# Performance work log

Measured on AMD Instinct MI355X. Metric: run time of the kernel, lower is better.

## Reference

```python
import jax, jax.numpy as jnp
import numpy as np
import math

D = 1024
H = 16
DH = D // H


def sinusoidal_pe(length, d):
    pos = jnp.arange(length, dtype=jnp.float32)[:, None]            # [S,1]
    div = jnp.exp(jnp.arange(0, d, 2, dtype=jnp.float32) * (-math.log(10000.0) / d))  # [d/2]
    ang = pos * div                                                  # [S,d/2]
    # interleave sin (even idx) and cos (odd idx)
    return jnp.stack([jnp.sin(ang), jnp.cos(ang)], axis=-1).reshape(length, d)


def setup_inputs() -> dict:
    key = jax.random.key(0)
    ks = jax.random.split(key, 12)
    s = 0.02
    x = jax.random.normal(ks[0], (2, 2048, D), dtype=jnp.float32)
    return {
        "x": x,
        "ln_g": jnp.ones((D,), jnp.float32),
        "ln_b": jnp.zeros((D,), jnp.float32),
        "Wq": jax.random.normal(ks[1], (D, D), jnp.float32) * s,
        "bq": jnp.zeros((D,), jnp.float32),
        "Wk": jax.random.normal(ks[2], (D, D), jnp.float32) * s,
        "bk": jnp.zeros((D,), jnp.float32),
        "Wv": jax.random.normal(ks[3], (D, D), jnp.float32) * s,
        "bv": jnp.zeros((D,), jnp.float32),
        "Wp": jax.random.normal(ks[4], (D, D), jnp.float32) * s,
        "Wo": jax.random.normal(ks[5], (D, D), jnp.float32) * s,
        "bo": jnp.zeros((D,), jnp.float32),
        "u_bias": jax.random.normal(ks[6], (H, DH), jnp.float32) * 0.05,
        "v_bias": jax.random.normal(ks[7], (H, DH), jnp.float32) * 0.05,
    }


def _relative_shift(pos_score):
    # pos_score: [B,H,S,S]
    B, Hh, S1, S2 = pos_score.shape
    padded = jnp.concatenate([jnp.zeros((B, Hh, S1, 1), pos_score.dtype), pos_score], axis=-1)
    padded = padded.reshape(B, Hh, S2 + 1, S1)
    return padded[:, :, 1:].reshape(B, Hh, S1, S2)


def reference(x, ln_g, ln_b, Wq, bq, Wk, bk, Wv, bv, Wp, Wo, bo, u_bias, v_bias):
    B, S, Dm = x.shape
    dh = Dm // H
    scale = dh ** -0.5

    pe = sinusoidal_pe(S, Dm)                                        # [S,D]

    mu = jnp.mean(x, axis=-1, keepdims=True)
    var = jnp.var(x, axis=-1, keepdims=True)
    xn = (x - mu) / jnp.sqrt(var + 1e-5) * ln_g + ln_b

    q = (xn @ Wq + bq).reshape(B, S, H, dh)                          # [B,S,H,dh]
    k = (xn @ Wk + bk).reshape(B, S, H, dh)
    v = (xn @ Wv + bv).reshape(B, S, H, dh)
    p = (pe @ Wp).reshape(S, H, dh)                                  # [S,H,dh]

    content = jnp.einsum('bihd,bjhd->bhij', q + u_bias, k)
    pos = jnp.einsum('bihd,jhd->bhij', q + v_bias, p)
    pos = _relative_shift(pos)

    attn = jax.nn.softmax((content + pos) * scale, axis=-1)          # [B,H,S,S]
    head = jnp.einsum('bhij,bjhd->bihd', attn, v).reshape(B, S, Dm)
    return head @ Wo + bo
```

## Files before the change

kernel.cpp:

```cpp
#include <hip/hip_runtime.h>
#include <hip/hip_bf16.h>
#include <math.h>

#define Dm   1024
#define Hh   16
#define Sx   2048

typedef short s16x8 __attribute__((ext_vector_type(8)));
typedef float f32x4 __attribute__((ext_vector_type(4)));
typedef unsigned short u16;
typedef u16 u16x4 __attribute__((ext_vector_type(4)));

#if defined(__has_builtin)
#  if __has_builtin(__builtin_amdgcn_cvt_pk_bf16_f32)
#    define HAVE_PKBF16 1
typedef __bf16 bfv2 __attribute__((ext_vector_type(2)));
#  endif
#  if __has_builtin(__builtin_amdgcn_exp2f)
#    define EXP2(x) __builtin_amdgcn_exp2f(x)
#  endif
#endif
#ifndef EXP2
#  define EXP2(x) exp2f(x)
#endif

#define ATT_SCALE 0.1803368801111204f

#define BARRIER_LGKM() asm volatile("s_waitcnt lgkmcnt(0)\n\ts_barrier" ::: "memory")

__device__ __forceinline__ float wave_sum64(float v) {
#pragma unroll
    for (int o = 32; o > 0; o >>= 1) v += __shfl_xor(v, o, 64);
    return v;
}
__device__ __forceinline__ u16 f2bf(float x) {
    unsigned int u = __float_as_uint(x);
    unsigned int r = u + 0x7FFFu + ((u >> 16) & 1u);
    return (u16)(r >> 16);
}
__device__ __forceinline__ float bf2f(u16 h) {
    return __uint_as_float(((unsigned int)h) << 16);
}
__device__ __forceinline__ f32x4 mfma16(s16x8 a, s16x8 b, f32x4 c) {
    return __builtin_amdgcn_mfma_f32_16x16x32_bf16(a, b, c, 0, 0, 0);
}
__device__ __forceinline__ void gl16(const u16* gp, u16* lp) {
    __builtin_amdgcn_global_load_lds(
        (__attribute__((address_space(1))) void*)(gp),
        (__attribute__((address_space(3))) void*)(lp), 16, 0, 0);
}

__global__ __launch_bounds__(256) void ln_kernel(const float* __restrict__ x,
                                                 const float* __restrict__ g,
                                                 const float* __restrict__ b,
                                                 u16* __restrict__ out16) {
    int row = blockIdx.x;
    int tid = threadIdx.x;
    const float4* xr = (const float4*)(x + (size_t)row * Dm);
    float4 v = xr[tid];
    float s  = v.x + v.y + v.z + v.w;
    float ss = v.x * v.x + v.y * v.y + v.z * v.z + v.w * v.w;
    __shared__ float rbuf[8];
    s  = wave_sum64(s);
    ss = wave_sum64(ss);
    if ((tid & 63) == 0) { rbuf[tid >> 6] = s; rbuf[4 + (tid >> 6)] = ss; }
    __syncthreads();
    float mean = (rbuf[0] + rbuf[1] + rbuf[2] + rbuf[3]) * (1.0f / Dm);
    float msq  = (rbuf[4] + rbuf[5] + rbuf[6] + rbuf[7]) * (1.0f / Dm);
    float var  = msq - mean * mean;
    float rstd = 1.0f / sqrtf(var + 1e-5f);
    float4 gg = ((const float4*)g)[tid];
    float4 bb = ((const float4*)b)[tid];
    float o[4];
    o[0] = (v.x - mean) * rstd * gg.x + bb.x;
    o[1] = (v.y - mean) * rstd * gg.y + bb.y;
    o[2] = (v.z - mean) * rstd * gg.z + bb.z;
    o[3] = (v.w - mean) * rstd * gg.w + bb.w;
    u16x4 hi, lo;
#pragma unroll
    for (int i = 0; i < 4; i++) {
        u16 h = f2bf(o[i]);
        hi[i] = h;
        lo[i] = f2bf(o[i] - bf2f(h));
    }
    *(u16x4*)&out16[(size_t)row * 2048 + tid * 4]        = hi;
    *(u16x4*)&out16[(size_t)row * 2048 + 1024 + tid * 4] = lo;
}

__global__ __launch_bounds__(256) void pe_kernel(u16* __restrict__ pe16) {
    int idx = blockIdx.x * 256 + threadIdx.x;
    int r = idx >> 9;
    int t = idx & 511;
    float div = expf((float)(2 * t) * (-9.210340371976184f / 1024.0f));
    float ang = (float)r * div;
    float sv, cv;
    sincosf(ang, &sv, &cv);
    u16 sh = f2bf(sv), chh = f2bf(cv);
    u16* row = pe16 + (size_t)r * 2048;
    row[2 * t]            = sh;
    row[2 * t + 1]        = chh;
    row[1024 + 2 * t]     = f2bf(sv - bf2f(sh));
    row[1024 + 2 * t + 1] = f2bf(cv - bf2f(chh));
}

__global__ __launch_bounds__(256) void wconv_kernel(const float* __restrict__ W0,
                                                    const float* __restrict__ W1,
                                                    const float* __restrict__ W2,
                                                    const float* __restrict__ W3,
                                                    const float* __restrict__ W4,
                                                    u16* __restrict__ WT) {
    int wz = blockIdx.z;
    const float* W = (wz == 0) ? W0 : (wz == 1) ? W1 : (wz == 2) ? W2 : (wz == 3) ? W3 : W4;
    u16* T = WT + (size_t)wz * 1024 * 2048;
    __shared__ float tile[32][33];
    int n0 = blockIdx.x * 32, k0 = blockIdx.y * 32;
    int tx = threadIdx.x & 31, ty = threadIdx.x >> 5;
#pragma unroll
    for (int r = 0; r < 32; r += 8)
        tile[ty + r][tx] = W[(size_t)(k0 + ty + r) * 1024 + n0 + tx];
    __syncthreads();
#pragma unroll
    for (int r = 0; r < 32; r += 8) {
        int n = ty + r;
        float x = tile[tx][n];
        u16 h = f2bf(x);
        float rem = x - bf2f(h);
        T[(size_t)(n0 + n) * 2048 + k0 + tx]        = h;
        T[(size_t)(n0 + n) * 2048 + 1024 + k0 + tx] = f2bf(rem);
    }
}

template<int BMT>
__global__ __launch_bounds__(256, 4) void gemm128k(const u16* __restrict__ A,
                                                   const u16* __restrict__ A2,
                                                   const u16* __restrict__ WT,
                                                   const float* __restrict__ b0,
                                                   const float* __restrict__ b1,
                                                   const float* __restrict__ b2,
                                                   const float* __restrict__ ubv,
                                                   const float* __restrict__ vbv,
                                                   float* __restrict__ ukg,
                                                   float* __restrict__ vbg,
                                                   u16* __restrict__ Cb,
                                                   u16* __restrict__ VT,
                                                   float* __restrict__ C,
                                                   int mode) {
    constexpr int MT  = BMT / 32;
    constexpr int AC  = BMT / 32;
    constexpr int RPW = BMT / 4;
    __shared__ __align__(16) u16 AhL[BMT * 64];
    __shared__ __align__(16) u16 BhL[128 * 64];
    int tid = threadIdx.x;
    int gx, gy, widx;
    const u16* Asrc = A;
    if (mode == 0) {
        int bid = blockIdx.x;
        if (bid < 768) { gx = bid % 24; gy = bid / 24; widx = gx >> 3; gx &= 7; }
        else           { int r2 = bid - 768; gx = r2 & 7; gy = r2 >> 3; widx = 3; Asrc = A2; }
    } else {
        gx = blockIdx.x; gy = blockIdx.y; widx = 4;
    }
    int bn = gx * 128, bm = gy * BMT;
    const u16* Wb = WT + (size_t)widx * (1024 * 2048);
    const float* bias = (widx == 0) ? b0 : (widx == 1) ? b1 : (widx == 2) ? b2
                      : (widx == 4) ? b0 : nullptr;
    float csc = (widx == 1 || widx == 3) ? ATT_SCALE : 1.0f;

    int w = tid >> 6, ln = tid & 63, g = ln >> 4, l15 = ln & 15;
    int wm = (w & 1) * (BMT / 2), wn = (w >> 1) * 64;

    int key = ln >> 3;
    int cg  = (ln & 7) ^ key;
    int gcol = (cg < 4) ? cg * 8 : 1024 + (cg - 4) * 8;
    const u16* gA = Asrc + (size_t)(bm + w * RPW + key) * 2048 + gcol;
    const u16* gB = Wb   + (size_t)(bn + w * 32  + key) * 2048 + gcol;
    u16* lA = &AhL[(w * RPW) * 64];
    u16* lB = &BhL[(w * 32) * 64];

    int keyr = l15 & 7;
    int chH = (g ^ keyr) * 8;
    int chL = ((4 + g) ^ keyr) * 8;

    f32x4 acc[MT][4] = {};

    for (int k0 = 0; k0 < 1024; k0 += 32) {
#pragma unroll
        for (int c = 0; c < AC; c++)
            gl16(gA + c * (8 * 2048) + k0, lA + c * (8 * 64));
#pragma unroll
        for (int c = 0; c < 4; c++)
            gl16(gB + c * (8 * 2048) + k0, lB + c * (8 * 64));
        __syncthreads();

        s16x8 bhf[4], blf[4];
#pragma unroll
        for (int nt = 0; nt < 4; nt++) {
            int br = (wn + nt * 16 + l15) * 64;
            bhf[nt] = *(const s16x8*)&BhL[br + chH];
            blf[nt] = *(const s16x8*)&BhL[br + chL];
        }
#pragma unroll
        for (int mt = 0; mt < MT; mt++) {
            int ar = (wm + mt * 16 + l15) * 64;
            s16x8 ah = *(const s16x8*)&AhL[ar + chH];
            s16x8 al = *(const s16x8*)&AhL[ar + chL];
#pragma unroll
            for (int nt = 0; nt < 4; nt++) {
                acc[mt][nt] = mfma16(ah, bhf[nt], acc[mt][nt]);
                acc[mt][nt] = mfma16(al, bhf[nt], acc[mt][nt]);
                acc[mt][nt] = mfma16(ah, blf[nt], acc[mt][nt]);
            }
        }
        __syncthreads();
    }

    float bv4[4];
#pragma unroll
    for (int nt = 0; nt < 4; nt++)
        bv4[nt] = bias ? bias[bn + wn + nt * 16 + l15] : 0.0f;
    if (mode == 0) {
        if (widx == 2) {
            int bb  = bm >> 11;
            int hh  = (bn + wn) >> 6;
            int jt0 = ((bm & 2047) + wm) >> 5;
            int jr0 = g * 4;
#pragma unroll
            for (int mt = 0; mt < MT; mt++) {
#pragma unroll
                for (int nt = 0; nt < 4; nt++) {
                    u16x4 ov;
#pragma unroll
                    for (int r = 0; r < 4; r++)
                        ov[r] = f2bf(acc[mt][nt][r] + bv4[nt]);
                    int jt = jt0 + (mt >> 1);
                    int d  = 16 * nt + l15;
                    u16* dst = VT + ((size_t)(bb * 16 + hh) * 64 + jt) * 2048
                                  + d * 32 + (mt & 1) * 16 + jr0;
                    *(u16x4*)dst = ov;
                }
            }
        } else {
            u16* Co = Cb + (size_t)widx * (4096 * 1024);
            bool dored = (widx == 1 || widx == 3);
            int hh = (bn + wn) >> 6;
            float u4[4] = {0.f, 0.f, 0.f, 0.f};
            if (dored) {
                const float* uv = (widx == 1) ? ubv : vbv;
#pragma unroll
                for (int nt = 0; nt < 4; nt++) u4[nt] = uv[hh * 64 + 16 * nt + l15];
            }
#pragma unroll
            for (int mt = 0; mt < MT; mt++)
#pragma unroll
                for (int r = 0; r < 4; r++) {
                    int row = bm + wm + mt * 16 + g * 4 + r;
                    u16* cp = Co + (size_t)row * 1024 + bn + wn + l15;
                    u16 hv[4];
#pragma unroll
                    for (int nt = 0; nt < 4; nt++) {
                        hv[nt] = f2bf((acc[mt][nt][r] + bv4[nt]) * csc);
                        cp[16 * nt] = hv[nt];
                    }
                    if (dored) {
                        float s = bf2f(hv[0]) * u4[0] + bf2f(hv[1]) * u4[1]
                                + bf2f(hv[2]) * u4[2] + bf2f(hv[3]) * u4[3];
#pragma unroll
                        for (int o = 1; o < 16; o <<= 1) s += __shfl_xor(s, o, 64);
                        if (l15 == 0) {
                            if (widx == 1)
                                ukg[((size_t)((bm >> 11) * 16 + hh)) * 2048
                                    + ((bm & 2047) + wm + mt * 16 + g * 4 + r)] = s;
                            else
                                vbg[(size_t)hh * 2048 + (bm + wm + mt * 16 + g * 4 + r)] = s;
                        }
                    }
                }
        }
    } else {
#pragma unroll
        for (int mt = 0; mt < MT; mt++)
#pragma unroll
            for (int r = 0; r < 4; r++) {
                int row = bm + wm + mt * 16 + g * 4 + r;
                float* cp = C + (size_t)row * 1024 + bn + wn + l15;
#pragma unroll
                for (int nt = 0; nt < 4; nt++)
                    cp[16 * nt] = acc[mt][nt][r] + bv4[nt];
            }
    }
}

__device__ __forceinline__ void wfill2(s16x8 a0, s16x8 a1, const u16* PW,
                                       int g, int l15, f32x4& d0, f32x4& d1) {
    f32x4 z = {0.f, 0.f, 0.f, 0.f};
    s16x8 b00 = *(const s16x8*)&PW[l15 * 72 + g * 8];
    s16x8 b01 = *(const s16x8*)&PW[l15 * 72 + 32 + g * 8];
    s16x8 b10 = *(const s16x8*)&PW[(16 + l15) * 72 + g * 8];
    s16x8 b11 = *(const s16x8*)&PW[(16 + l15) * 72 + 32 + g * 8];
    d0 = mfma16(a0, b00, z);
    d0 = mfma16(a1, b01, d0);
    d1 = mfma16(a0, b10, z);
    d1 = mfma16(a1, b11, d1);
}

__device__ __forceinline__ void window_fill(s16x8 aq0, s16x8 aq1, s16x8 ab0, s16x8 ab1,
                                            const u16* PW, float* Ws,
                                            const float* __restrict__ vbb,
                                            int vstart, int sb, int rbase, int g, int l15) {
    f32x4 e0, e1;
    if (vstart + 31 <= Sx) {
        wfill2(aq0, aq1, PW, g, l15, e0, e1);
    } else if (vstart > Sx) {
        wfill2(ab0, ab1, PW, g, l15, e0, e1);
    } else {
        f32x4 d0, d1, f0, f1;
        wfill2(aq0, aq1, PW, g, l15, d0, d1);
        wfill2(ab0, ab1, PW, g, l15, f0, f1);
        int v0 = vstart + l15, v1 = vstart + 16 + l15;
#pragma unroll
        for (int r = 0; r < 4; r++) {
            e0[r] = (v0 > Sx) ? f0[r] : d0[r];
            e1[r] = (v1 > Sx) ? f1[r] : d1[r];
        }
    }
    int v0 = vstart + l15, v1 = vstart + 16 + l15;
    int pc0 = v0 < Sx ? v0 : v0 - Sx - 1;
    int pc1 = v1 < Sx ? v1 : v1 - Sx - 1;
    float vb0 = (v0 == Sx) ? 0.0f : vbb[pc0];
    float vb1 = (v1 == Sx) ? 0.0f : vbb[pc1];
    int bs = sb + rbase;
#pragma unroll
    for (int r = 0; r < 4; r++) {
        int b2 = bs + r; if (b2 >= 96) b2 -= 96;
        int sl0 = b2 + l15; if (sl0 >= 96) sl0 -= 96;
        int sl1 = sl0 + 16; if (sl1 >= 96) sl1 -= 96;
        Ws[(rbase + r) * 98 + sl0] = (v0 == Sx) ? 0.0f : e0[r] + vb0;
        Ws[(rbase + r) * 98 + sl1] = (v1 == Sx) ? 0.0f : e1[r] + vb1;
    }
}

__global__ __launch_bounds__(256, 4) void flash_kernel(const u16* __restrict__ q,
                                                       const u16* __restrict__ k,
                                                       const u16* __restrict__ vt,
                                                       const u16* __restrict__ pp,
                                                       const float* __restrict__ ukg,
                                                       const float* __restrict__ vbg,
                                                       u16* __restrict__ head16) {
    __shared__ __align__(16) unsigned char smem[39424];
    float* Ws = (float*)smem;
    u16*   Qs = (u16*)smem;
    u16*   Kt = (u16*)(smem + 25088);
    u16*   PW = (u16*)(smem + 29696);
    u16*   PA = (u16*)(smem + 34304);

    int tid = threadIdx.x, blk = blockIdx.x;
    int grp = (blk & 7) + 8 * (blk >> 8);
    int it  = (blk >> 3) & 31;
    int h = grp & 15, b = grp >> 4;
    int i0 = it * 64;
    int a0 = 1984 - i0;

    const u16* qb  = q  + ((size_t)b * Sx) * Dm + h * 64;
    const u16* kb  = k  + ((size_t)b * Sx) * Dm + h * 64;
    const u16* vtb = vt + ((size_t)(b * 16 + h) * 64) * 2048;
    const u16* ppb = pp + h * 64;
    const float* ukb = ukg + (size_t)(b * Hh + h) * Sx;
    const float* vbb = vbg + (size_t)h * Sx;

    int w = tid >> 6, ln = tid & 63, g = ln >> 4, l15 = ln & 15;
    int rv = tid >> 3, ch = tid & 7;
    int rbase = 16 * w + 4 * g;

    for (int c = tid; c < 65 * 8; c += 256) {
        int row = c >> 3, cc = c & 7;
        int i = i0 + row;
        s16x8 tv = {0, 0, 0, 0, 0, 0, 0, 0};
        if (i < Sx) tv = *(const s16x8*)(qb + (size_t)i * Dm + cc * 8);
        *(s16x8*)&Qs[row * 72 + cc * 8] = tv;
    }
    __syncthreads();

    s16x8 aq0 = *(const s16x8*)&Qs[(16 * w + l15) * 72 + g * 8];
    s16x8 aq1 = *(const s16x8*)&Qs[(16 * w + l15) * 72 + 32 + g * 8];
    s16x8 ab0 = *(const s16x8*)&Qs[(16 * w + 1 + l15) * 72 + g * 8];
    s16x8 ab1 = *(const s16x8*)&Qs[(16 * w + 1 + l15) * 72 + 32 + g * 8];
    __syncthreads();

    for (int f = 0; f < 3; f++) {
        int vrb = f * 32;
        if (f) __syncthreads();
        {
            int vv = a0 + vrb + rv;
            s16x8 tv = {0, 0, 0, 0, 0, 0, 0, 0};
            if (vv != Sx) {
                int pc = vv < Sx ? vv : vv - Sx - 1;
                tv = *(const s16x8*)(ppb + (size_t)pc * Dm + ch * 8);
            }
            *(s16x8*)&PW[rv * 72 + ch * 8] = tv;
        }
        __syncthreads();
        window_fill(aq0, aq1, ab0, ab1, PW, Ws, vbb, a0 + vrb, vrb, rbase, g, l15);
    }

    f32x4 O[4] = {{0.f,0.f,0.f,0.f},{0.f,0.f,0.f,0.f},{0.f,0.f,0.f,0.f},{0.f,0.f,0.f,0.f}};
    float m_w = -1e30f;
    float l_i[4] = {0.f, 0.f, 0.f, 0.f};
    int wro[4];
#pragma unroll
    for (int r = 0; r < 4; r++) wro[r] = (rbase + r) * 98;
    int sb = 0;
    int jm = 63;
    int cw = (g >= 2) ? 16 : 0;
    int crd = (l15 >> 3) << 4;
    int pard = (16 * w + l15) * 40 + ((g * 8 + crd) & 31);

    const u16* pK = kb + (size_t)rv * Dm + ch * 8;
    const u16* pV = vtb + l15 * 32 + g * 8;
    s16x8 rK = *(const s16x8*)pK;
    s16x8 rPW = {0, 0, 0, 0, 0, 0, 0, 0};

    for (int t = 0; t < 64; t++) {
        int j0 = t * 32;
        BARRIER_LGKM();
        *(s16x8*)&Kt[rv * 72 + ch * 8] = rK;
        if (t >= 1) *(s16x8*)&PW[rv * 72 + ch * 8] = rPW;

        s16x8 bv0 = *(const s16x8*)(pV);
        s16x8 bv1 = *(const s16x8*)(pV + 512);
        s16x8 bv2 = *(const s16x8*)(pV + 1024);
        s16x8 bv3 = *(const s16x8*)(pV + 1536);
        pV += 2048;

        pK += 32 * Dm;
        rK = *(const s16x8*)pK;
        {
            int vv = a0 + (t + 3) * 32 + rv;
            s16x8 z8 = {0, 0, 0, 0, 0, 0, 0, 0};
            if (vv != Sx) {
                int pc = vv < Sx ? vv : vv - Sx - 1;
                if (pc > Sx - 1) pc = Sx - 1;
                z8 = *(const s16x8*)(ppb + (size_t)pc * Dm + ch * 8);
            }
            rPW = z8;
        }
        float uk0 = ukb[j0 + l15];
        float uk1 = ukb[j0 + 16 + l15];
        BARRIER_LGKM();

        f32x4 s0, s1;
        {
            f32x4 z = {0.f, 0.f, 0.f, 0.f};
            s16x8 bk00 = *(const s16x8*)&Kt[l15 * 72 + g * 8];
            s16x8 bk01 = *(const s16x8*)&Kt[l15 * 72 + 32 + g * 8];
            s16x8 bk10 = *(const s16x8*)&Kt[(16 + l15) * 72 + g * 8];
            s16x8 bk11 = *(const s16x8*)&Kt[(16 + l15) * 72 + 32 + g * 8];
            s0 = mfma16(aq0, bk00, z);
            s0 = mfma16(aq1, bk01, s0);
            s1 = mfma16(aq0, bk10, z);
            s1 = mfma16(aq1, bk11, s1);
        }

        if (t >= 1) {
            window_fill(aq0, aq1, ab0, ab1, PW, Ws, vbb, a0 + j0 + 64, sb, rbase, g, l15);
            sb += 32; if (sb >= 96) sb -= 96;
        }

        int si0 = jm + l15; if (si0 >= 96) si0 -= 96;
        int si1 = si0 + 16; if (si1 >= 96) si1 -= 96;
        jm += 32; if (jm >= 96) jm -= 96;
        float lg0[4], lg1[4];
#pragma unroll
        for (int r = 0; r < 4; r++) {
            lg0[r] = s0[r] + uk0 + Ws[wro[r] + si0];
            lg1[r] = s1[r] + uk1 + Ws[wro[r] + si1];
        }
        float pmax = fmaxf(fmaxf(fmaxf(lg0[0], lg1[0]), fmaxf(lg0[1], lg1[1])),
                           fmaxf(fmaxf(lg0[2], lg1[2]), fmaxf(lg0[3], lg1[3])));
        if (__any(pmax > m_w + 8.0f)) {
            float mx = pmax;
#pragma unroll
            for (int o = 1; o < 64; o <<= 1) mx = fmaxf(mx, __shfl_xor(mx, o, 64));
            float alpha = EXP2(m_w - mx);
            m_w = mx;
            l_i[0] *= alpha; l_i[1] *= alpha; l_i[2] *= alpha; l_i[3] *= alpha;
#pragma unroll
            for (int nt = 0; nt < 4; nt++)
#pragma unroll
                for (int r = 0; r < 4; r++) O[nt][r] *= alpha;
        }
        int c0 = l15 + cw;
        int c1 = l15 + 16 - cw;
#pragma unroll
        for (int r = 0; r < 4; r++) {
            float e0v = EXP2(lg0[r] - m_w);
            float e1v = EXP2(lg1[r] - m_w);
            l_i[r] += e0v + e1v;
#ifdef HAVE_PKBF16
            bfv2 pk2 = __builtin_amdgcn_cvt_pk_bf16_f32(e0v, e1v);
            PA[(rbase + r) * 40 + c0] = __builtin_bit_cast(u16, pk2[0]);
            PA[(rbase + r) * 40 + c1] = __builtin_bit_cast(u16, pk2[1]);
#else
            PA[(rbase + r) * 40 + c0] = f2bf(e0v);
            PA[(rbase + r) * 40 + c1] = f2bf(e1v);
#endif
        }

        {
            s16x8 ap = *(const s16x8*)&PA[pard];
            O[0] = mfma16(ap, bv0, O[0]);
            O[1] = mfma16(ap, bv1, O[1]);
            O[2] = mfma16(ap, bv2, O[2]);
            O[3] = mfma16(ap, bv3, O[3]);
        }
    }

#pragma unroll
    for (int r = 0; r < 4; r++) {
        float l = l_i[r];
#pragma unroll
        for (int o = 1; o < 16; o <<= 1) l += __shfl_xor(l, o, 64);
        float inv = 1.0f / l;
        int grow = i0 + rbase + r;
        u16* dst = head16 + (size_t)(b * Sx + grow) * 2048 + h * 64 + l15;
#pragma unroll
        for (int nt = 0; nt < 4; nt++) {
            float f = O[nt][r] * inv;
            u16 hh = f2bf(f);
            dst[16 * nt]        = hh;
            dst[1024 + 16 * nt] = f2bf(f - bf2f(hh));
        }
    }
}

extern "C" void kernel_launch(void* const* d_in, const int* in_sizes, int n_in,
                              void* d_out, int out_size, void* d_ws, size_t ws_size,
                              hipStream_t stream) {
    const float* x    = (const float*)d_in[0];
    const float* ln_g = (const float*)d_in[1];
    const float* ln_b = (const float*)d_in[2];
    const float* Wq   = (const float*)d_in[3];
    const float* bq   = (const float*)d_in[4];
    const float* Wk   = (const float*)d_in[5];
    const float* bk   = (const float*)d_in[6];
    const float* Wv   = (const float*)d_in[7];
    const float* bv   = (const float*)d_in[8];
    const float* Wp   = (const float*)d_in[9];
    const float* Wo   = (const float*)d_in[10];
    const float* bo   = (const float*)d_in[11];
    const float* ub   = (const float*)d_in[12];
    const float* vbias= (const float*)d_in[13];

    float* out = (float*)d_out;
    u16* base  = (u16*)d_ws;

    const int MROWS = 2 * Sx;
    u16* xn16   = base;
    u16* head16 = base + 8u  * 1024 * 1024;
    u16* pe16   = base + 16u * 1024 * 1024;
    u16* qb16   = base + 20u * 1024 * 1024;
    u16* kb16   = base + 24u * 1024 * 1024;
    u16* pp16   = base + 32u * 1024 * 1024;
    u16* vT16   = base + 34u * 1024 * 1024;
    u16* WT     = base + 38u * 1024 * 1024;
    float* ukg  = (float*)(base + 48u * 1024 * 1024);
    float* vbg  = ukg + 2 * Hh * Sx;
    (void)kb16; (void)pp16;

    ln_kernel<<<MROWS, 256, 0, stream>>>(x, ln_g, ln_b, xn16);
    pe_kernel<<<Sx * 512 / 256, 256, 0, stream>>>(pe16);

    dim3 gw(32, 32, 5);
    wconv_kernel<<<gw, 256, 0, stream>>>(Wq, Wk, Wv, Wp, Wo, WT);

    gemm128k<128><<<896, 256, 0, stream>>>(xn16, pe16, WT, bq, bk, bv,
                                           ub, vbias, ukg, vbg,
                                           qb16, vT16, nullptr, 0);

    flash_kernel<<<2 * Hh * 32, 256, 0, stream>>>(qb16, kb16, vT16, pp16, ukg, vbg, head16);

    gemm128k<64><<<dim3(8, 64), 256, 0, stream>>>(head16, nullptr, WT, bo, nullptr, nullptr,
                                                  nullptr, nullptr, nullptr, nullptr,
                                                  nullptr, nullptr, out, 1);
}
```

Measured before the change: 368.0 us.

## Merge prep kernels into one launch and add dedicated 64x64 output GEMM

Folds the LayerNorm, positional-encoding and weight-transpose kernels into one prep kernel that dispatches on block index, removing two launches. Replaces the templated output projection with a dedicated 64x64-tile GEMM that uses direct global-to-LDS loads, swizzled LDS, and three bf16 MFMAs per step (hi*hi, lo*hi, hi*lo). The launch now has 1024 blocks instead of 512. The flash kernel's custom lgkmcnt barrier is swapped for __syncthreads, which may add extra waits for outstanding memory operations.

```diff
diff --git a/kernel.cpp b/kernel.cpp
--- a/kernel.cpp
+++ b/kernel.cpp
@@ -26,8 +26,6 @@
 
 #define ATT_SCALE 0.1803368801111204f
 
-#define BARRIER_LGKM() asm volatile("s_waitcnt lgkmcnt(0)\n\ts_barrier" ::: "memory")
-
 __device__ __forceinline__ float wave_sum64(float v) {
 #pragma unroll
     for (int o = 32; o > 0; o >>= 1) v += __shfl_xor(v, o, 64);
@@ -50,83 +48,86 @@
         (__attribute__((address_space(3))) void*)(lp), 16, 0, 0);
 }
 
-__global__ __launch_bounds__(256) void ln_kernel(const float* __restrict__ x,
-                                                 const float* __restrict__ g,
-                                                 const float* __restrict__ b,
-                                                 u16* __restrict__ out16) {
-    int row = blockIdx.x;
+__global__ __launch_bounds__(256) void prep_kernel(const float* __restrict__ x,
+                                                   const float* __restrict__ g,
+                                                   const float* __restrict__ b,
+                                                   u16* __restrict__ out16,
+                                                   u16* __restrict__ pe16,
+                                                   const float* __restrict__ W0,
+                                                   const float* __restrict__ W1,
+                                                   const float* __restrict__ W2,
+                                                   const float* __restrict__ W3,
+                                                   const float* __restrict__ W4,
+                                                   u16* __restrict__ WT) {
+    __shared__ float rbuf[8];
+    __shared__ float tile[32][33];
+    int bid = blockIdx.x;
     int tid = threadIdx.x;
-    const float4* xr = (const float4*)(x + (size_t)row * Dm);
-    float4 v = xr[tid];
-    float s  = v.x + v.y + v.z + v.w;
-    float ss = v.x * v.x + v.y * v.y + v.z * v.z + v.w * v.w;
-    __shared__ float rbuf[8];
-    s  = wave_sum64(s);
-    ss = wave_sum64(ss);
-    if ((tid & 63) == 0) { rbuf[tid >> 6] = s; rbuf[4 + (tid >> 6)] = ss; }
-    __syncthreads();
-    float mean = (rbuf[0] + rbuf[1] + rbuf[2] + rbuf[3]) * (1.0f / Dm);
-    float msq  = (rbuf[4] + rbuf[5] + rbuf[6] + rbuf[7]) * (1.0f / Dm);
-    float var  = msq - mean * mean;
-    float rstd = 1.0f / sqrtf(var + 1e-5f);
-    float4 gg = ((const float4*)g)[tid];
-    float4 bb = ((const float4*)b)[tid];
-    float o[4];
-    o[0] = (v.x - mean) * rstd * gg.x + bb.x;
-    o[1] = (v.y - mean) * rstd * gg.y + bb.y;
-    o[2] = (v.z - mean) * rstd * gg.z + bb.z;
-    o[3] = (v.w - mean) * rstd * gg.w + bb.w;
-    u16x4 hi, lo;
-#pragma unroll
-    for (int i = 0; i < 4; i++) {
-        u16 h = f2bf(o[i]);
-        hi[i] = h;
-        lo[i] = f2bf(o[i] - bf2f(h));
-    }
-    *(u16x4*)&out16[(size_t)row * 2048 + tid * 4]        = hi;
-    *(u16x4*)&out16[(size_t)row * 2048 + 1024 + tid * 4] = lo;
-}
-
-__global__ __launch_bounds__(256) void pe_kernel(u16* __restrict__ pe16) {
-    int idx = blockIdx.x * 256 + threadIdx.x;
-    int r = idx >> 9;
-    int t = idx & 511;
-    float div = expf((float)(2 * t) * (-9.210340371976184f / 1024.0f));
-    float ang = (float)r * div;
-    float sv, cv;
-    sincosf(ang, &sv, &cv);
-    u16 sh = f2bf(sv), chh = f2bf(cv);
-    u16* row = pe16 + (size_t)r * 2048;
-    row[2 * t]            = sh;
-    row[2 * t + 1]        = chh;
-    row[1024 + 2 * t]     = f2bf(sv - bf2f(sh));
-    row[1024 + 2 * t + 1] = f2bf(cv - bf2f(chh));
-}
-
-__global__ __launch_bounds__(256) void wconv_kernel(const float* __restrict__ W0,
-                                                    const float* __restrict__ W1,
-                                                    const float* __restrict__ W2,
-                                                    const float* __restrict__ W3,
-                                                    const float* __restrict__ W4,
-                                                    u16* __restrict__ WT) {
-    int wz = blockIdx.z;
-    const float* W = (wz == 0) ? W0 : (wz == 1) ? W1 : (wz == 2) ? W2 : (wz == 3) ? W3 : W4;
-    u16* T = WT + (size_t)wz * 1024 * 2048;
-    __shared__ float tile[32][33];
-    int n0 = blockIdx.x * 32, k0 = blockIdx.y * 32;
-    int tx = threadIdx.x & 31, ty = threadIdx.x >> 5;
-#pragma unroll
-    for (int r = 0; r < 32; r += 8)
-        tile[ty + r][tx] = W[(size_t)(k0 + ty + r) * 1024 + n0 + tx];
-    __syncthreads();
-#pragma unroll
-    for (int r = 0; r < 32; r += 8) {
-        int n = ty + r;
-        float x = tile[tx][n];
-        u16 h = f2bf(x);
-        float rem = x - bf2f(h);
-        T[(size_t)(n0 + n) * 2048 + k0 + tx]        = h;
-        T[(size_t)(n0 + n) * 2048 + 1024 + k0 + tx] = f2bf(rem);
+    if (bid < 4096) {
+        int row = bid;
+        const float4* xr = (const float4*)(x + (size_t)row * Dm);
+        float4 v = xr[tid];
+        float s  = v.x + v.y + v.z + v.w;
+        float ss = v.x * v.x + v.y * v.y + v.z * v.z + v.w * v.w;
+        s  = wave_sum64(s);
+        ss = wave_sum64(ss);
+        if ((tid & 63) == 0) { rbuf[tid >> 6] = s; rbuf[4 + (tid >> 6)] = ss; }
+        __syncthreads();
+        float mean = (rbuf[0] + rbuf[1] + rbuf[2] + rbuf[3]) * (1.0f / Dm);
+        float msq  = (rbuf[4] + rbuf[5] + rbuf[6] + rbuf[7]) * (1.0f / Dm);
+        float var  = msq - mean * mean;
+        float rstd = 1.0f / sqrtf(var + 1e-5f);
+        float4 gg = ((const float4*)g)[tid];
+        float4 bb = ((const float4*)b)[tid];
+        float o[4];
+        o[0] = (v.x - mean) * rstd * gg.x + bb.x;
+        o[1] = (v.y - mean) * rstd * gg.y + bb.y;
+        o[2] = (v.z - mean) * rstd * gg.z + bb.z;
+        o[3] = (v.w - mean) * rstd * gg.w + bb.w;
+        u16x4 hi, lo;
+#pragma unroll
+        for (int i = 0; i < 4; i++) {
+            u16 h = f2bf(o[i]);
+            hi[i] = h;
+            lo[i] = f2bf(o[i] - bf2f(h));
+        }
+        *(u16x4*)&out16[(size_t)row * 2048 + tid * 4]        = hi;
+        *(u16x4*)&out16[(size_t)row * 2048 + 1024 + tid * 4] = lo;
+    } else if (bid < 8192) {
+        int idx = (bid - 4096) * 256 + tid;
+        int r = idx >> 9;
+        int t = idx & 511;
+        float div = expf((float)(2 * t) * (-9.210340371976184f / 1024.0f));
+        float ang = (float)r * div;
+        float sv, cv;
+        sincosf(ang, &sv, &cv);
+        u16 sh = f2bf(sv), chh = f2bf(cv);
+        u16* row = pe16 + (size_t)r * 2048;
+        row[2 * t]            = sh;
+        row[2 * t + 1]        = chh;
+        row[1024 + 2 * t]     = f2bf(sv - bf2f(sh));
+        row[1024 + 2 * t + 1] = f2bf(cv - bf2f(chh));
+    } else {
+        int r0 = bid - 8192;
+        int wz = r0 >> 10;
+        int rem = r0 & 1023;
+        int n0 = (rem & 31) * 32, k0 = (rem >> 5) * 32;
+        const float* W = (wz == 0) ? W0 : (wz == 1) ? W1 : (wz == 2) ? W2 : (wz == 3) ? W3 : W4;
+        u16* T = WT + (size_t)wz * 1024 * 2048;
+        int tx = tid & 31, ty = tid >> 5;
+#pragma unroll
+        for (int r = 0; r < 32; r += 8)
+            tile[ty + r][tx] = W[(size_t)(k0 + ty + r) * 1024 + n0 + tx];
+        __syncthreads();
+#pragma unroll
+        for (int r = 0; r < 32; r += 8) {
+            int n = ty + r;
+            float xv = tile[tx][n];
+            u16 h = f2bf(xv);
+            float rem2 = xv - bf2f(h);
+            T[(size_t)(n0 + n) * 2048 + k0 + tx]        = h;
+            T[(size_t)(n0 + n) * 2048 + 1024 + k0 + tx] = f2bf(rem2);
+        }
     }
 }
 
@@ -290,6 +291,80 @@
     }
 }
 
+__global__ __launch_bounds__(256, 4) void gemm64(const u16* __restrict__ A,
+                                                 const u16* __restrict__ WT,
+                                                 const float* __restrict__ bias,
+                                                 float* __restrict__ C) {
+    __shared__ __align__(16) u16 AhL[64 * 64];
+    __shared__ __align__(16) u16 BhL[64 * 64];
+    int tid = threadIdx.x;
+    int bn = blockIdx.x * 64, bm = blockIdx.y * 64;
+    const u16* Wb = WT + (size_t)4 * (1024 * 2048);
+
+    int w = tid >> 6, ln = tid & 63, g = ln >> 4, l15 = ln & 15;
+    int wm = (w & 1) * 32, wn = (w >> 1) * 32;
+
+    int key = ln >> 3;
+    int cg  = (ln & 7) ^ key;
+    int gcol = (cg < 4) ? cg * 8 : 1024 + (cg - 4) * 8;
+    const u16* gA = A  + (size_t)(bm + w * 8 + key) * 2048 + gcol;
+    const u16* gB = Wb + (size_t)(bn + w * 8 + key) * 2048 + gcol;
+    u16* lA = &AhL[(w * 8) * 64];
+    u16* lB = &BhL[(w * 8) * 64];
+
+    int keyr = l15 & 7;
+    int chH = (g ^ keyr) * 8;
+    int chL = ((4 + g) ^ keyr) * 8;
+
+    f32x4 acc[2][2] = {};
+
+    for (int k0 = 0; k0 < 1024; k0 += 32) {
+#pragma unroll
+        for (int c = 0; c < 2; c++)
+            gl16(gA + c * (32 * 2048) + k0, lA + c * (32 * 64));
+#pragma unroll
+        for (int c = 0; c < 2; c++)
+            gl16(gB + c * (32 * 2048) + k0, lB + c * (32 * 64));
+        __syncthreads();
+
+        s16x8 bhf[2], blf[2];
+#pragma unroll
+        for (int nt = 0; nt < 2; nt++) {
+            int br = (wn + nt * 16 + l15) * 64;
+            bhf[nt] = *(const s16x8*)&BhL[br + chH];
+            blf[nt] = *(const s16x8*)&BhL[br + chL];
+        }
+#pragma unroll
+        for (int mt = 0; mt < 2; mt++) {
+            int ar = (wm + mt * 16 + l15) * 64;
+            s16x8 ah = *(const s16x8*)&AhL[ar + chH];
+            s16x8 al = *(const s16x8*)&AhL[ar + chL];
+#pragma unroll
+            for (int nt = 0; nt < 2; nt++) {
+                acc[mt][nt] = mfma16(ah, bhf[nt], acc[mt][nt]);
+                acc[mt][nt] = mfma16(al, bhf[nt], acc[mt][nt]);
+                acc[mt][nt] = mfma16(ah, blf[nt], acc[mt][nt]);
+            }
+        }
+        __syncthreads();
+    }
+
+    float bv2[2];
+#pragma unroll
+    for (int nt = 0; nt < 2; nt++)
+        bv2[nt] = bias[bn + wn + nt * 16 + l15];
+#pragma unroll
+    for (int mt = 0; mt < 2; mt++)
+#pragma unroll
+        for (int r = 0; r < 4; r++) {
+            int row = bm + wm + mt * 16 + g * 4 + r;
+            float* cp = C + (size_t)row * 1024 + bn + wn + l15;
+#pragma unroll
+            for (int nt = 0; nt < 2; nt++)
+                cp[16 * nt] = acc[mt][nt][r] + bv2[nt];
+        }
+}
+
 __device__ __forceinline__ void wfill2(s16x8 a0, s16x8 a1, const u16* PW,
                                        int g, int l15, f32x4& d0, f32x4& d1) {
     f32x4 z = {0.f, 0.f, 0.f, 0.f};
@@ -421,7 +496,7 @@
 
     for (int t = 0; t < 64; t++) {
         int j0 = t * 32;
-        BARRIER_LGKM();
+        __syncthreads();
         *(s16x8*)&Kt[rv * 72 + ch * 8] = rK;
         if (t >= 1) *(s16x8*)&PW[rv * 72 + ch * 8] = rPW;
 
@@ -445,7 +520,7 @@
         }
         float uk0 = ukb[j0 + l15];
         float uk1 = ukb[j0 + 16 + l15];
-        BARRIER_LGKM();
+        __syncthreads();
 
         f32x4 s0, s1;
         {
@@ -553,7 +628,6 @@
     float* out = (float*)d_out;
     u16* base  = (u16*)d_ws;
 
-    const int MROWS = 2 * Sx;
     u16* xn16   = base;
     u16* head16 = base + 8u  * 1024 * 1024;
     u16* pe16   = base + 16u * 1024 * 1024;
@@ -564,13 +638,9 @@
     u16* WT     = base + 38u * 1024 * 1024;
     float* ukg  = (float*)(base + 48u * 1024 * 1024);
     float* vbg  = ukg + 2 * Hh * Sx;
-    (void)kb16; (void)pp16;
-
-    ln_kernel<<<MROWS, 256, 0, stream>>>(x, ln_g, ln_b, xn16);
-    pe_kernel<<<Sx * 512 / 256, 256, 0, stream>>>(pe16);
-
-    dim3 gw(32, 32, 5);
-    wconv_kernel<<<gw, 256, 0, stream>>>(Wq, Wk, Wv, Wp, Wo, WT);
+
+    prep_kernel<<<13312, 256, 0, stream>>>(x, ln_g, ln_b, xn16, pe16,
+                                           Wq, Wk, Wv, Wp, Wo, WT);
 
     gemm128k<128><<<896, 256, 0, stream>>>(xn16, pe16, WT, bq, bk, bv,
                                            ub, vbias, ukg, vbg,
@@ -578,7 +648,5 @@
 
     flash_kernel<<<2 * Hh * 32, 256, 0, stream>>>(qb16, kb16, vT16, pp16, ukg, vbg, head16);
 
-    gemm128k<64><<<dim3(8, 64), 256, 0, stream>>>(head16, nullptr, WT, bo, nullptr, nullptr,
-                                                  nullptr, nullptr, nullptr, nullptr,
-                                                  nullptr, nullptr, out, 1);
-}
+    gemm64<<<dim3(16, 64), 256, 0, stream>>>(head16, WT, bo, out);
+}
```

New measurement: 371.6 us. About the same (+1.0%).
